# Kernel tuning notes

Measured on AMD Instinct MI355X. Metric: run time of the kernel, lower is better.

## Reference

```python
import jax, jax.numpy as jnp
import numpy as np

T, B, S, D = 512, 32, 512, 512
EPS = 1e-6  # LayerNorm eps


def _ln(x, g, b):
    m = jnp.mean(x, axis=-1, keepdims=True)
    v = jnp.mean((x - m) ** 2, axis=-1, keepdims=True)
    return g * (x - m) * jax.lax.rsqrt(v + EPS) + b


def setup_inputs() -> dict:
    key = jax.random.key(0)
    ks = jax.random.split(key, 10)
    sc = 1.0 / np.sqrt(D).astype(np.float32)
    return {
        "prev_layer": jax.random.normal(ks[0], (T, B, D), jnp.float32),
        "hidden": jax.random.normal(ks[1], (B, D), jnp.float32),
        "enc_output": jax.random.normal(ks[2], (B, S, D), jnp.float32),
        "memory_length": jax.random.randint(ks[3], (B,), 1, S + 1),
        # nn.Linear weights stored as [in, out] (transposed torch layout)
        "W_in": jax.random.normal(ks[4], (D, 3 * D), jnp.float32) * sc,
        "W_enc": jax.random.normal(ks[5], (D, D), jnp.float32) * sc,
        "W_attn_in": jax.random.normal(ks[6], (D, D), jnp.float32) * sc,
        "W_hidden": jax.random.normal(ks[7], (D, D), jnp.float32) * sc,
        "W_ctx": jax.random.normal(ks[8], (D, D), jnp.float32) * sc,
        # LayerNorm gains/biases (5 LNs)
        "g_pre": jnp.ones((3 * D,), jnp.float32), "b_pre": jnp.zeros((3 * D,), jnp.float32),
        "g_enc": jnp.ones((D,), jnp.float32), "b_enc": jnp.zeros((D,), jnp.float32),
        "g_attn": jnp.ones((D,), jnp.float32), "b_attn": jnp.zeros((D,), jnp.float32),
        "g_h": jnp.ones((D,), jnp.float32), "b_h": jnp.zeros((D,), jnp.float32),
        "g_c": jnp.ones((D,), jnp.float32), "b_c": jnp.zeros((D,), jnp.float32),
    }


def reference(prev_layer, hidden, enc_output, W_in, W_enc, W_attn_in, W_hidden,
              W_ctx, g_pre, b_pre, g_enc, b_enc, g_attn, b_attn, g_h, b_h,
              g_c, b_c, memory_length):
    d = prev_layer.shape[-1]
    sqrt_d = jnp.sqrt(jnp.asarray(d, prev_layer.dtype))
    # dropout is identity in eval mode
    preact = _ln(prev_layer @ W_in, g_pre, b_pre)          # [T,B,3D]
    pctx = _ln(enc_output @ W_enc, g_enc, b_enc)           # [B,S,D]
    z, h_gate, pl_t = jnp.split(preact, 3, axis=-1)
    z = jax.nn.sigmoid(z)
    h_gate = jax.nn.sigmoid(h_gate)

    # SRU-style linear recurrence: s_t = (1-z_t)*s_{t-1} + z_t*pl_t
    def step(h, zp):
        z_t, p_t = zp
        s = (1.0 - z_t) * h + z_t * p_t
        return s, s

    hidden_last, ss = jax.lax.scan(step, hidden, (z, pl_t))  # ss: [T,B,D]

    attn_in = _ln(ss @ W_attn_in, g_attn, b_attn)            # [T,B,D]
    align = jnp.einsum('tbd,bsd->bts', attn_in, pctx)        # [B,T,S]
    mask = jnp.arange(pctx.shape[1])[None, :] < memory_length[:, None]  # [B,S]
    align = jnp.where(mask[:, None, :], align, -jnp.inf)
    av = jax.nn.softmax(align / sqrt_d, axis=-1)             # [B,T,S]
    c = jnp.einsum('bts,bsd->tbd', av, pctx)                 # [T,B,D]
    attn_out = c / sqrt_d

    trans = _ln(ss @ W_hidden, g_h, b_h) + _ln(attn_out @ W_ctx, g_c, b_c)
    out = jnp.tanh(trans)
    out = (1.0 - h_gate) * out + h_gate * prev_layer         # [T,B,D]
    p_attn = jnp.transpose(av, (1, 0, 2))                    # [T,B,S]
    return out, hidden_last, p_attn
```

## Files before the change

### kernel.cpp

```cpp
#include <hip/hip_runtime.h>
#include <hip/hip_bf16.h>
#include <cmath>

#define T_ 512
#define B_ 32
#define S_ 512
#define D_ 512
#define NCH 16
#define CT (T_ / NCH)
static constexpr float LN_EPS = 1e-6f;
static constexpr float RSQRT_D = 0.044194173824159216f;

typedef __attribute__((ext_vector_type(8))) __bf16 bf16x8;
typedef __attribute__((ext_vector_type(4))) float f32x4;

struct __align__(8) bfx4 { __hip_bfloat16 x, y, z, w; };
struct __align__(16) u16x8 { unsigned short h[8]; };

__device__ __forceinline__ void g2l16(const void* g, void* l) {
    __builtin_amdgcn_global_load_lds(
        (const __attribute__((address_space(1))) unsigned int*)g,
        (__attribute__((address_space(3))) unsigned int*)l, 16, 0, 0);
}

__device__ __forceinline__ float xr_sum16(float v) {
    v += __shfl_xor(v, 1); v += __shfl_xor(v, 2);
    v += __shfl_xor(v, 4); v += __shfl_xor(v, 8); return v;
}
__device__ __forceinline__ float xr_max16(float v) {
    v = fmaxf(v, __shfl_xor(v, 1)); v = fmaxf(v, __shfl_xor(v, 2));
    v = fmaxf(v, __shfl_xor(v, 4)); v = fmaxf(v, __shfl_xor(v, 8)); return v;
}

__device__ __forceinline__ float sigmoidf_(float x) {
    return 1.f / (1.f + __expf(-x));
}
__device__ __forceinline__ float sigmoid_fast(float x) {
    return __fdividef(1.f, 1.f + __expf(-x));
}
__device__ __forceinline__ float tanh_fast(float x) {
    return 1.f - __fdividef(2.f, __expf(2.f * x) + 1.f);
}
__device__ __forceinline__ float bfu(unsigned short u) {
    unsigned int v = ((unsigned int)u) << 16;
    return __uint_as_float(v);
}
__device__ __forceinline__ unsigned short f2bu(float f) {
    return __hip_bfloat16_raw(__float2bfloat16(f)).x;
}

__device__ __forceinline__ void g128_body(
    const __hip_bfloat16* __restrict__ A, long ldaE,
    const __hip_bfloat16* __restrict__ Bw,
    __hip_bfloat16* __restrict__ out, long outStrideB,
    float2* __restrict__ part, int partMul, int partBase,
    float scale, int bx, int by)
{
    __shared__ char smem[32768];
    const int m0 = by * 128, n0 = bx * 128;
    const int tid = threadIdx.x, lane = tid & 63, w = tid >> 6;
    const int wm = (w >> 1) * 64, wn = (w & 1) * 64;
    const int srow = lane >> 2, skB = (lane & 3) * 16;
    const int q = lane >> 4, c = lane & 15;

    f32x4 acc[4][4];
#pragma unroll
    for (int i = 0; i < 4; i++)
#pragma unroll
        for (int j = 0; j < 4; j++) acc[i][j] = (f32x4)(0.0f);

    const char* ga0 = (const char*)(A + (long)(m0 + w * 16 + srow) * ldaE) + skB;
    const char* ga1 = (const char*)(A + (long)(m0 + (w + 4) * 16 + srow) * ldaE) + skB;
    const char* gb0 = (const char*)(Bw + (long)(n0 + w * 16 + srow) * 512) + skB;
    const char* gb1 = (const char*)(Bw + (long)(n0 + (w + 4) * 16 + srow) * 512) + skB;
    char* la0 = smem + w * 1024 + lane * 16;
    char* la1 = smem + (w + 4) * 1024 + lane * 16;
    char* lb0 = smem + 8192 + w * 1024 + lane * 16;
    char* lb1 = smem + 8192 + (w + 4) * 1024 + lane * 16;
    const char* Ar = smem + (wm + c) * 64 + q * 16;
    const char* Br = smem + 8192 + (wn + c) * 64 + q * 16;

    g2l16(ga0, la0);
    g2l16(ga1, la1);
    g2l16(gb0, lb0);
    g2l16(gb1, lb1);
    __syncthreads();

#pragma unroll
    for (int kk = 0; kk < 16; kk++) {
        const int cb = (kk & 1) << 14;
        const int nb = cb ^ 16384;
        if (kk < 15) {
            const long kb = (long)(kk + 1) * 64;
            g2l16(ga0 + kb, la0 + nb);
            g2l16(ga1 + kb, la1 + nb);
            g2l16(gb0 + kb, lb0 + nb);
            g2l16(gb1 + kb, lb1 + nb);
        }
        bf16x8 af[4], bfr[4];
#pragma unroll
        for (int i = 0; i < 4; i++) {
            af[i] = *(const bf16x8*)(Ar + cb + i * 1024);
            bfr[i] = *(const bf16x8*)(Br + cb + i * 1024);
        }
#pragma unroll
        for (int i = 0; i < 4; i++)
#pragma unroll
            for (int j = 0; j < 4; j++)
                acc[i][j] = __builtin_amdgcn_mfma_f32_16x16x32_bf16(
                    af[i], bfr[j], acc[i][j], 0, 0, 0);
        __syncthreads();
    }

    if (part) {
        float2* sred = (float2*)smem;
#pragma unroll
        for (int i = 0; i < 4; i++)
#pragma unroll
            for (int r = 0; r < 4; r++) {
                float s = 0.f, qq = 0.f;
#pragma unroll
                for (int j = 0; j < 4; j++) {
                    float v = acc[i][j][r] * scale; s += v; qq += v * v;
                }
                s = xr_sum16(s); qq = xr_sum16(qq);
                if (c == 0) sred[(wm + i * 16 + q * 4 + r) * 2 + (w & 1)] =
                    make_float2(s, qq);
            }
        __syncthreads();
        if ((w & 1) == 0 && c == 0) {
#pragma unroll
            for (int i = 0; i < 4; i++)
#pragma unroll
                for (int r = 0; r < 4; r++) {
                    int row = wm + i * 16 + q * 4 + r;
                    float2 a = sred[row * 2], b2 = sred[row * 2 + 1];
                    part[(long)bx * 16384 + (long)(m0 + row) * partMul + partBase] =
                        make_float2(a.x + b2.x, a.y + b2.y);
                }
        }
        __syncthreads();
    }

    for (int p = 0; p < 2; p++) {
        if ((w >> 1) == p) {
#pragma unroll
            for (int i = 0; i < 4; i++)
#pragma unroll
                for (int j = 0; j < 4; j++)
#pragma unroll
                    for (int r = 0; r < 4; r++) {
                        int row = i * 16 + q * 4 + r;
                        int col = wn + j * 16 + c;
                        ((__hip_bfloat16*)smem)[row * 128 + col] =
                            __float2bfloat16(acc[i][j][r] * scale);
                    }
        }
        __syncthreads();
#pragma unroll
        for (int rnd = 0; rnd < 4; rnd++) {
            int row = rnd * 16 + (tid >> 4);
            int ch = tid & 15;
            uint4 v = *(const uint4*)(smem + row * 256 + ch * 16);
            long grow = m0 + p * 64 + row;
            *(uint4*)((char*)out + grow * outStrideB + (long)n0 * 2 + ch * 16) = v;
        }
        __syncthreads();
    }
}

__global__ __launch_bounds__(256) void g128(
    const __hip_bfloat16* __restrict__ A, long ldaE,
    const __hip_bfloat16* __restrict__ Bw, long bStrideZ,
    __hip_bfloat16* __restrict__ out, long outStrideB,
    float2* __restrict__ part, float scale, int swizzle)
{
    int bx, by, pmul = 1, pbase = 0;
    if (gridDim.z > 1) {
        const int bpz = gridDim.x * gridDim.y;
        const int nwg = bpz * gridDim.z;
        const int lin = (blockIdx.z * gridDim.y + blockIdx.y) * gridDim.x
                        + blockIdx.x;
        const int swz = (lin & 7) * (nwg >> 3) + (lin >> 3);
        const int z = swz / bpz, rem = swz % bpz;
        bx = rem % gridDim.x; by = rem / gridDim.x;
        A += (long)z * 512;
        Bw += (long)z * bStrideZ;
        out += (long)z * 512;
        pmul = 32; pbase = z;
    } else if (swizzle) {
        const int nwg = gridDim.x * gridDim.y;
        const int lin = blockIdx.y * gridDim.x + blockIdx.x;
        const int cpx = nwg >> 3;
        const int swz = (lin & 7) * cpx + (lin >> 3);
        bx = swz % gridDim.x; by = swz / gridDim.x;
    } else { bx = blockIdx.x; by = blockIdx.y; }
    g128_body(A, ldaE, Bw, out, outStrideB, part, pmul, pbase, scale, bx, by);
}

__global__ __launch_bounds__(256) void g128e2s(
    const __hip_bfloat16* __restrict__ encb,
    const __hip_bfloat16* __restrict__ WE2,
    __hip_bfloat16* __restrict__ E2, float2* __restrict__ partA,
    const __hip_bfloat16* __restrict__ preb, const float2* __restrict__ stats,
    const float* __restrict__ gpre, const float* __restrict__ bpre,
    float* __restrict__ Ap, float* __restrict__ Bp)
{
    const int bid = blockIdx.x;
    if (bid < 512) {
        int i2 = (bid & 31) * 256 + threadIdx.x;
        int b = i2 >> 8, d = (i2 & 255) * 2;
        int idx = b * 512 + d;
        int ch = bid >> 5;
        float2 gz = *(const float2*)(gpre + d), bz = *(const float2*)(bpre + d);
        float2 gp = *(const float2*)(gpre + 1024 + d);
        float2 bp = *(const float2*)(bpre + 1024 + d);
        float A0 = 1.f, s0 = 0.f, A1 = 1.f, s1 = 0.f;
        for (int t = ch * CT; t < (ch + 1) * CT; t++) {
            long row = (long)t * 32 + b;
            float2 st = stats[row];
            ushort2 zr = *(const ushort2*)(preb + row * 1536 + d);
            ushort2 pr = *(const ushort2*)(preb + row * 1536 + 1024 + d);
            float z0 = sigmoidf_((bfu(zr.x) - st.x) * st.y * gz.x + bz.x);
            float z1 = sigmoidf_((bfu(zr.y) - st.x) * st.y * gz.y + bz.y);
            float p0 = (bfu(pr.x) - st.x) * st.y * gp.x + bp.x;
            float p1 = (bfu(pr.y) - st.x) * st.y * gp.y + bp.y;
            A0 *= (1.f - z0); s0 = (1.f - z0) * s0 + z0 * p0;
            A1 *= (1.f - z1); s1 = (1.f - z1) * s1 + z1 * p1;
        }
        *(float2*)(Ap + ch * 16384 + idx) = make_float2(A0, A1);
        *(float2*)(Bp + ch * 16384 + idx) = make_float2(s0, s1);
        return;
    }
    const int local = bid - 512;
    const int swz = (local & 7) * 128 + (local >> 3);
    g128_body(encb, 512, WE2, E2, 2048, partA, 1, 0, 1.f, swz & 7, swz >> 3);
}

__global__ __launch_bounds__(256) void mfix3(
    const __hip_bfloat16* __restrict__ preb, const float2* __restrict__ stats,
    const float* __restrict__ gpre, const float* __restrict__ bpre,
    const float* __restrict__ sinb, __hip_bfloat16* __restrict__ ssb,
    const __hip_bfloat16* __restrict__ E2,
    __hip_bfloat16* __restrict__ pctxb, __hip_bfloat16* __restrict__ pwT,
    const float2* __restrict__ partA,
    const float* __restrict__ g, const float* __restrict__ bb,
    const float* __restrict__ uv)
{
    __shared__ __hip_bfloat16 t[32][34];
    __shared__ float2 sst[32];
    const int bid = blockIdx.x;
    if (bid < 512) {
        int i2 = (bid & 31) * 256 + threadIdx.x;
        int b = i2 >> 8, d = (i2 & 255) * 2;
        int idx = b * 512 + d;
        int ch = bid >> 5;
        float2 gz = *(const float2*)(gpre + d), bz = *(const float2*)(bpre + d);
        float2 gp = *(const float2*)(gpre + 1024 + d);
        float2 bp = *(const float2*)(bpre + 1024 + d);
        float2 sv = *(const float2*)(sinb + ch * 16384 + idx);
        float s0 = sv.x, s1 = sv.y;
        for (int tt = ch * CT; tt < (ch + 1) * CT; tt++) {
            long row = (long)tt * 32 + b;
            float2 st = stats[row];
            ushort2 zr = *(const ushort2*)(preb + row * 1536 + d);
            ushort2 pr = *(const ushort2*)(preb + row * 1536 + 1024 + d);
            float z0 = sigmoidf_((bfu(zr.x) - st.x) * st.y * gz.x + bz.x);
            float z1 = sigmoidf_((bfu(zr.y) - st.x) * st.y * gz.y + bz.y);
            float p0 = (bfu(pr.x) - st.x) * st.y * gp.x + bp.x;
            float p1 = (bfu(pr.y) - st.x) * st.y * gp.y + bp.y;
            s0 += z0 * (p0 - s0);
            s1 += z1 * (p1 - s1);
            ushort2 o;
            o.x = f2bu(s0); o.y = f2bu(s1);
            *(ushort2*)(ssb + (long)tt * 16384 + idx) = o;
        }
        return;
    }
    const int local = bid - 512;
    const int d0 = (local & 15) * 32;
    const int s0 = ((local >> 4) & 15) * 32;
    const int b = local >> 8;
    if (threadIdx.x < 32) {
        long row = (long)b * 512 + s0 + threadIdx.x;
        float s = 0.f, qq = 0.f;
#pragma unroll
        for (int cb = 0; cb < 4; cb++) {
            float2 v = partA[(long)cb * 16384 + row]; s += v.x; qq += v.y;
        }
        float mn = s * (1.f / 512);
        sst[threadIdx.x] =
            make_float2(mn, rsqrtf(qq * (1.f / 512) - mn * mn + LN_EPS));
    }
    __syncthreads();
    const int tx = threadIdx.x & 31, ty = threadIdx.x >> 5;
    const float gv = g[d0 + tx], bv = bb[d0 + tx];
    const float ud = uv[d0 + tx], vd = uv[512 + d0 + tx];
#pragma unroll
    for (int i = 0; i < 4; i++) {
        int srow = s0 + ty + i * 8;
        long row = (long)b * 512 + srow;
        float2 s = sst[ty + i * 8];
        float pc = __bfloat162float(E2[row * 1024 + d0 + tx]);
        pctxb[row * 512 + d0 + tx] =
            __float2bfloat16((pc - s.x) * s.y * gv + bv);
        float pr = __bfloat162float(E2[row * 1024 + 512 + d0 + tx]);
        t[ty + i * 8][tx] = __float2bfloat16(s.y * pr - s.y * s.x * ud + vd);
    }
    __syncthreads();
#pragma unroll
    for (int i = 0; i < 4; i++)
        pwT[(long)b * 262144 + (long)(d0 + ty + i * 8) * 512 + s0 + tx] =
            t[tx][ty + i * 8];
}

#define RC_BUF 34816
__global__ __launch_bounds__(256, 2) void gemm_attn(
    const __hip_bfloat16* __restrict__ attninC2,
    const __hip_bfloat16* __restrict__ pctxb,
    const float2* __restrict__ partB,
    const float* __restrict__ g_att, const float* __restrict__ b_att,
    const int* __restrict__ mlen,
    float* __restrict__ pattn, __hip_bfloat16* __restrict__ softb)
{
    __shared__ char smem[74240];
    float2* sst = (float2*)(smem + 69632);
    float* gln = (float*)(smem + 69888);
    float* bln = (float*)(smem + 71936);
    const int lin = blockIdx.z * 16 + blockIdx.y;
    const int swzb = (lin & 7) * 64 + (lin >> 3);
    const int b = swzb >> 4;
    const long t0 = (long)(swzb & 15) * 32;
    const int tid = threadIdx.x, lane = tid & 63, w = tid >> 6;

    if (tid < 32) {
        long grow = (t0 + tid) * 32 + b;
        float s = 0.f, qq = 0.f;
#pragma unroll
        for (int cb = 0; cb < 4; cb++) {
            float2 v = partB[(long)cb * 16384 + grow]; s += v.x; qq += v.y;
        }
        float mn = s * (1.f / 512);
        sst[tid] = make_float2(mn, rsqrtf(qq * (1.f / 512) - mn * mn + LN_EPS));
    }
    gln[tid] = g_att[tid]; gln[256 + tid] = g_att[256 + tid];
    bln[tid] = b_att[tid]; bln[256 + tid] = b_att[256 + tid];

    f32x4 acc[2][8];
#pragma unroll
    for (int m = 0; m < 2; m++)
#pragma unroll
        for (int j = 0; j < 8; j++) acc[m][j] = (f32x4)(0.0f);

    const __hip_bfloat16* A = attninC2 + (long)b * 1024 + t0 * 32768;
    const __hip_bfloat16* Bm = pctxb + (long)b * 262144;
    const char* ga = (const char*)(A + (long)(w * 16 + (lane >> 2)) * 32768) + (lane & 3) * 16;
    char* la = smem + w * 1024 + lane * 16;
    const char* gb = (const char*)(Bm + (long)(w * 128 + (lane >> 2)) * 512) + (lane & 3) * 16;
    char* lb = smem + 2048 + w * 8192 + lane * 16;
    const long ldbB16 = 512L * 32;
    const char* Ar = smem + (lane & 15) * 64 + (lane >> 4) * 16;
    const char* Br = smem + 2048 + (w * 128 + (lane & 15)) * 64 + (lane >> 4) * 16;

    if (w < 2) g2l16(ga, la);
#pragma unroll
    for (int s = 0; s < 8; s++) g2l16(gb + s * ldbB16, lb + s * 1024);
    __syncthreads();

    const int fr = lane & 15, kq = lane >> 4;
    const float2 st0 = sst[fr], st1 = sst[16 + fr];

#pragma unroll
    for (int kk = 0; kk < 16; kk++) {
        const int cb = (kk & 1) * RC_BUF;
        const int nb = ((kk & 1) ^ 1) * RC_BUF;
        if (kk < 15) {
            const long kb = (long)(kk + 1) * 64;
            if (w < 2) g2l16(ga + kb, la + nb);
#pragma unroll
            for (int s = 0; s < 8; s++)
                g2l16(gb + kb + s * ldbB16, lb + nb + s * 1024);
        }
        bf16x8 af[2], bfr[8];
#pragma unroll
        for (int m = 0; m < 2; m++) af[m] = *(const bf16x8*)(Ar + cb + m * 1024);
#pragma unroll
        for (int j = 0; j < 8; j++) bfr[j] = *(const bf16x8*)(Br + cb + j * 1024);
        {
            const int k0 = kk * 32 + kq * 8;
            float4 gq0 = *(const float4*)(gln + k0);
            float4 gq1 = *(const float4*)(gln + k0 + 4);
            float4 bq0 = *(const float4*)(bln + k0);
            float4 bq1 = *(const float4*)(bln + k0 + 4);
            float gj[8] = {gq0.x, gq0.y, gq0.z, gq0.w, gq1.x, gq1.y, gq1.z, gq1.w};
            float bj[8] = {bq0.x, bq0.y, bq0.z, bq0.w, bq1.x, bq1.y, bq1.z, bq1.w};
            u16x8 u0 = __builtin_bit_cast(u16x8, af[0]);
            u16x8 u1 = __builtin_bit_cast(u16x8, af[1]);
#pragma unroll
            for (int j = 0; j < 8; j++) {
                u0.h[j] = f2bu((bfu(u0.h[j]) - st0.x) * st0.y * gj[j] + bj[j]);
                u1.h[j] = f2bu((bfu(u1.h[j]) - st1.x) * st1.y * gj[j] + bj[j]);
            }
            af[0] = __builtin_bit_cast(bf16x8, u0);
            af[1] = __builtin_bit_cast(bf16x8, u1);
        }
#pragma unroll
        for (int m = 0; m < 2; m++)
#pragma unroll
            for (int j = 0; j < 8; j++)
                acc[m][j] = __builtin_amdgcn_mfma_f32_16x16x32_bf16(
                    af[m], bfr[j], acc[m][j], 0, 0, 0);
        __syncthreads();
    }

    const int q = lane >> 4, c = lane & 15;
    const int len = mlen[b];
    float* sred = (float*)smem;

#pragma unroll
    for (int m = 0; m < 2; m++)
#pragma unroll
        for (int r = 0; r < 4; r++) {
            float mx = -INFINITY;
#pragma unroll
            for (int j = 0; j < 8; j++) {
                int col = w * 128 + j * 16 + c;
                float v = acc[m][j][r] * RSQRT_D;
                acc[m][j][r] = v;
                if (col < len) mx = fmaxf(mx, v);
            }
            mx = xr_max16(mx);
            if (c == 0) sred[(m * 16 + q * 4 + r) * 4 + w] = mx;
        }
    __syncthreads();
    float rmax[2][4];
#pragma unroll
    for (int m = 0; m < 2; m++)
#pragma unroll
        for (int r = 0; r < 4; r++) {
            int row = m * 16 + q * 4 + r;
            rmax[m][r] = fmaxf(fmaxf(sred[row * 4], sred[row * 4 + 1]),
                               fmaxf(sred[row * 4 + 2], sred[row * 4 + 3]));
        }
    __syncthreads();
#pragma unroll
    for (int m = 0; m < 2; m++)
#pragma unroll
        for (int r = 0; r < 4; r++) {
            float s = 0.f;
#pragma unroll
            for (int j = 0; j < 8; j++) {
                int col = w * 128 + j * 16 + c;
                float e = (col < len) ? __expf(acc[m][j][r] - rmax[m][r]) : 0.f;
                acc[m][j][r] = e; s += e;
            }
            s = xr_sum16(s);
            if (c == 0) sred[(m * 16 + q * 4 + r) * 4 + w] = s;
        }
    __syncthreads();
    float rinv[2][4];
#pragma unroll
    for (int m = 0; m < 2; m++)
#pragma unroll
        for (int r = 0; r < 4; r++) {
            int row = m * 16 + q * 4 + r;
            rinv[m][r] = 1.f / (sred[row * 4] + sred[row * 4 + 1] +
                                sred[row * 4 + 2] + sred[row * 4 + 3]);
        }
    __syncthreads();

#pragma unroll
    for (int m = 0; m < 2; m++)
#pragma unroll
        for (int j = 0; j < 8; j++)
#pragma unroll
            for (int r = 0; r < 4; r++) {
                int row = m * 16 + q * 4 + r;
                int col = w * 128 + j * 16 + c;
                float p = acc[m][j][r] * rinv[m][r];
                pattn[((t0 + row) * 32 + b) * 512 + col] = p;
                ((__hip_bfloat16*)smem)[row * 512 + col] = __float2bfloat16(p);
            }
    __syncthreads();
#pragma unroll
    for (int rnd = 0; rnd < 8; rnd++) {
        int row = rnd * 4 + w;
        uint4 v = *(const uint4*)(smem + row * 1024 + lane * 16);
        *(uint4*)((char*)softb + ((t0 + row) * 32 + b) * 1024 + lane * 16) = v;
    }
}

__global__ __launch_bounds__(256) void fin_ep(
    const __hip_bfloat16* __restrict__ h2r,
    const __hip_bfloat16* __restrict__ C2,
    const __hip_bfloat16* __restrict__ preb,
    const float2* __restrict__ partC,
    const float2* __restrict__ partH,
    const float2* __restrict__ st_p,
    const float* __restrict__ g_c, const float* __restrict__ b_c,
    const float* __restrict__ g_h, const float* __restrict__ b_h,
    const float* __restrict__ g_pre, const float* __restrict__ b_pre,
    const float* __restrict__ prev, float* __restrict__ out)
{
    __shared__ float2 shc[32], shh[32];
    const long m0 = (long)blockIdx.x * 32;
    const int tid = threadIdx.x;
    if (tid < 32) {
        long rowg = m0 + tid;
        float s = 0.f, qq = 0.f;
#pragma unroll
        for (int cb = 0; cb < 4; cb++) {
            float2 v = partC[(long)cb * 16384 + rowg]; s += v.x; qq += v.y;
        }
        float mn = s * (1.f / 512);
        shc[tid] = make_float2(mn, rsqrtf(qq * (1.f / 512) - mn * mn + LN_EPS));
    } else if (tid < 64) {
        long rowg = m0 + tid - 32;
        float s = 0.f, qq = 0.f;
#pragma unroll
        for (int cb = 0; cb < 4; cb++) {
            float2 v = partH[(long)cb * 16384 + rowg]; s += v.x; qq += v.y;
        }
        float mn = s * (1.f / 512);
        shh[tid - 32] = make_float2(mn, rsqrtf(qq * (1.f / 512) - mn * mn + LN_EPS));
    }
    __syncthreads();
#pragma unroll
    for (int ch = 0; ch < 16; ch++) {
        int f4 = ch * 256 + tid;
        int row = f4 >> 7;
        long rowg = m0 + row;
        int col = (f4 & 127) * 4;
        ushort4 h2 = *(const ushort4*)((const char*)h2r + rowg * 1024 + col * 2);
        ushort4 h1 = *(const ushort4*)((const char*)C2 + rowg * 2048 + 1024 + col * 2);
        ushort4 hr = *(const ushort4*)((const char*)preb + rowg * 3072 + 1024 + col * 2);
        float4 pv = *(const float4*)(prev + rowg * 512 + col);
        float4 gc = *(const float4*)(g_c + col), bc = *(const float4*)(b_c + col);
        float4 gh = *(const float4*)(g_h + col), bh = *(const float4*)(b_h + col);
        float4 gp = *(const float4*)(g_pre + 512 + col);
        float4 bp = *(const float4*)(b_pre + 512 + col);
        float2 sc = shc[row], sh = shh[row], sp = st_p[rowg];
        auto fuse = [&](unsigned short h2u, unsigned short h1u, unsigned short hru,
                        float pvv, float gcv, float bcv, float ghv, float bhv,
                        float gpv, float bpv) -> float {
            float t2 = (bfu(h2u) - sc.x) * sc.y * gcv + bcv;
            float t1 = (bfu(h1u) - sh.x) * sh.y * ghv + bhv;
            float hg = sigmoid_fast((bfu(hru) - sp.x) * sp.y * gpv + bpv);
            return (1.f - hg) * tanh_fast(t1 + t2) + hg * pvv;
        };
        float4 o;
        o.x = fuse(h2.x, h1.x, hr.x, pv.x, gc.x, bc.x, gh.x, bh.x, gp.x, bp.x);
        o.y = fuse(h2.y, h1.y, hr.y, pv.y, gc.y, bc.y, gh.y, bh.y, gp.y, bp.y);
        o.z = fuse(h2.z, h1.z, hr.z, pv.z, gc.z, bc.z, gh.z, bh.z, gp.z, bp.z);
        o.w = fuse(h2.w, h1.w, hr.w, pv.w, gc.w, bc.w, gh.w, bh.w, gp.w, bp.w);
        *(float4*)(out + rowg * 512 + col) = o;
    }
}

__global__ __launch_bounds__(256) void cvt4d(
    const float* __restrict__ a, __hip_bfloat16* __restrict__ ya,
    const float* __restrict__ b, __hip_bfloat16* __restrict__ yb)
{
    int i = blockIdx.x * 256 + threadIdx.x;
    const float* x; __hip_bfloat16* y; int k;
    if (i < 2097152) { x = a; y = ya; k = i; }
    else { x = b; y = yb; k = i - 2097152; }
    float4 v = ((const float4*)x)[k];
    bfx4 o;
    o.x = __float2bfloat16(v.x); o.y = __float2bfloat16(v.y);
    o.z = __float2bfloat16(v.z); o.w = __float2bfloat16(v.w);
    ((bfx4*)y)[k] = o;
}

__global__ __launch_bounds__(256) void wtrans(
    const float* __restrict__ w0, const float* __restrict__ w1,
    const float* __restrict__ w2, const float* __restrict__ w3,
    const float* __restrict__ w4, __hip_bfloat16* __restrict__ WT,
    __hip_bfloat16* __restrict__ WE2)
{
    int z = blockIdx.z;
    const float* W; __hip_bfloat16* O; int N;
    if (z == 0)      { W = w0; O = WT;                          N = 1536; }
    else if (z == 1) { W = w1; O = WE2;                         N = 512; }
    else if (z == 2) { W = w2; O = WT + 786432 + 262144;        N = 512; }
    else if (z == 3) { W = w3; O = WT + 786432 + 524288;        N = 512; }
    else             { W = w4; O = WT + 786432 + 786432;        N = 512; }
    int n0 = blockIdx.x * 32, k0 = blockIdx.y * 32;
    if (n0 >= N) return;
    __shared__ float t[32][33];
    int tx = threadIdx.x & 31, ty = threadIdx.x >> 5;
#pragma unroll
    for (int i = 0; i < 4; i++)
        t[ty + i * 8][tx] = W[(long)(k0 + ty + i * 8) * N + n0 + tx];
    __syncthreads();
#pragma unroll
    for (int i = 0; i < 4; i++)
        O[(long)(n0 + ty + i * 8) * 512 + k0 + tx] =
            __float2bfloat16(t[tx][ty + i * 8]);
}

__global__ __launch_bounds__(256) void wprep(
    const __hip_bfloat16* __restrict__ wctxT, const float* __restrict__ g,
    __hip_bfloat16* __restrict__ wgT,
    const float* __restrict__ Wenc, __hip_bfloat16* __restrict__ wencb,
    const float* __restrict__ Wctx, const float* __restrict__ bvec,
    float* __restrict__ uv)
{
    const int bid = blockIdx.x;
    if (bid < 1024) {
        int i = bid * 256 + threadIdx.x;
        int d1 = i & 511;
        wgT[i] = __float2bfloat16(__bfloat162float(wctxT[i]) * g[d1]);
    } else if (bid < 1280) {
        int i = (bid - 1024) * 256 + threadIdx.x;
        float4 v = ((const float4*)Wenc)[i];
        bfx4 o;
        o.x = __float2bfloat16(v.x); o.y = __float2bfloat16(v.y);
        o.z = __float2bfloat16(v.z); o.w = __float2bfloat16(v.w);
        ((bfx4*)wencb)[i] = o;
    } else {
        int d = (bid - 1280) * 256 + threadIdx.x;
        float u = 0.f, v = 0.f;
        for (int k = 0; k < 512; k++) {
            float w = Wctx[(long)k * 512 + d];
            u += g[k] * w; v += bvec[k] * w;
        }
        uv[d] = u; uv[512 + d] = v;
    }
}

__global__ __launch_bounds__(256) void stats_fin(
    const float2* __restrict__ part, float2* __restrict__ stats)
{
    int r = blockIdx.x * 256 + threadIdx.x;
    float s = 0.f, qq = 0.f;
#pragma unroll
    for (int cb = 0; cb < 12; cb++) {
        float2 v = part[(long)cb * 16384 + r]; s += v.x; qq += v.y;
    }
    float m = s * (1.f / 1536);
    float rs = rsqrtf(qq * (1.f / 1536) - m * m + LN_EPS);
    stats[r] = make_float2(m, rs);
}

__global__ __launch_bounds__(256) void scan_part2(
    const float* __restrict__ Ap, const float* __restrict__ Bp,
    const float* __restrict__ h0, float* __restrict__ sin_,
    float* __restrict__ hlast)
{
    int idx = blockIdx.x * 256 + threadIdx.x;
    float s = h0[idx];
    for (int ch = 0; ch < NCH; ch++) {
        sin_[ch * 16384 + idx] = s;
        s = Ap[ch * 16384 + idx] * s + Bp[ch * 16384 + idx];
    }
    hlast[idx] = s;
}

extern "C" void kernel_launch(void* const* d_in, const int* in_sizes, int n_in,
                              void* d_out, int out_size, void* d_ws, size_t ws_size,
                              hipStream_t stream) {
    const float* prev  = (const float*)d_in[0];
    const float* hid0  = (const float*)d_in[1];
    const float* enc   = (const float*)d_in[2];
    const int*   mlen  = (const int*)  d_in[3];
    const float* W_in  = (const float*)d_in[4];
    const float* W_enc = (const float*)d_in[5];
    const float* W_att = (const float*)d_in[6];
    const float* W_hid = (const float*)d_in[7];
    const float* W_ctx = (const float*)d_in[8];
    const float* g_pre = (const float*)d_in[9];
    const float* b_pre = (const float*)d_in[10];
    const float* g_enc = (const float*)d_in[11];
    const float* b_enc = (const float*)d_in[12];
    const float* g_att = (const float*)d_in[13];
    const float* b_att = (const float*)d_in[14];
    const float* g_h   = (const float*)d_in[15];
    const float* b_h   = (const float*)d_in[16];
    const float* g_c   = (const float*)d_in[17];
    const float* b_c   = (const float*)d_in[18];

    float* out   = (float*)d_out;
    float* hlast = out + (long)T_ * B_ * D_;
    float* pattn = hlast + (long)B_ * D_;

    char* ws = (char*)d_ws;
    __hip_bfloat16* preb    = (__hip_bfloat16*)(ws);
    __hip_bfloat16* WT      = (__hip_bfloat16*)(ws + 50331648);
    __hip_bfloat16* prevb   = (__hip_bfloat16*)(ws + 54525952);
    __hip_bfloat16* encb    = (__hip_bfloat16*)(ws + 71303168);
    __hip_bfloat16* pctxb   = (__hip_bfloat16*)(ws + 88080384);
    __hip_bfloat16* pwT     = (__hip_bfloat16*)(ws + 104857600);
    __hip_bfloat16* ssb     = (__hip_bfloat16*)(ws + 121634816);
    __hip_bfloat16* C2      = (__hip_bfloat16*)(ws + 138412032);
    __hip_bfloat16* E2      = (__hip_bfloat16*)(ws + 171966464);
    __hip_bfloat16* softb   = (__hip_bfloat16*)(ws + 171966464);
    __hip_bfloat16* h2raw   = (__hip_bfloat16*)(ws + 188743680);
    float2* part            = (float2*)(ws + 205520896);
    float2* stats           = (float2*)(ws + 207618048);
    float* scanA            = (float*)(ws + 207749120);
    float* scanB            = (float*)(ws + 208797696);
    float* sinb             = (float*)(ws + 209846272);
    __hip_bfloat16* WE2     = (__hip_bfloat16*)(ws + 211419136);
    float* uv               = (float*)(ws + 212467712);
    __hip_bfloat16* WgT     = (__hip_bfloat16*)scanA;
    __hip_bfloat16* Wencbf  = (__hip_bfloat16*)scanB;

    float2* partA = part;
    float2* partB = part + 8 * 16384;
    float2* partC = part;

    const __hip_bfloat16* W_attT = WT + 786432 + 262144;
    const __hip_bfloat16* W_ctxT = WT + 786432 + 786432;

    dim3 blk(256);

    cvt4d<<<16384, blk, 0, stream>>>(prev, prevb, enc, encb);
    wtrans<<<dim3(48, 16, 5), blk, 0, stream>>>(W_in, W_enc, W_att, W_hid,
                                                W_ctx, WT, WE2);
    wprep<<<1282, blk, 0, stream>>>(W_ctxT, g_enc, WgT, W_enc, Wencbf,
                                    W_ctx, b_enc, uv);
    g128<<<dim3(4, 4), blk, 0, stream>>>(WgT, 512, Wencbf, 0, WE2 + 262144,
                                         1024, nullptr, 1.f, 0);

    g128<<<dim3(12, 128), blk, 0, stream>>>(prevb, 512, WT, 0, preb, 3072,
                                            part, 1.f, 1);
    stats_fin<<<64, blk, 0, stream>>>(part, stats);

    g128e2s<<<1536, blk, 0, stream>>>(encb, WE2, E2, partA, preb, stats,
                                      g_pre, b_pre, scanA, scanB);
    scan_part2<<<64, blk, 0, stream>>>(scanA, scanB, hid0, sinb, hlast);

    mfix3<<<8704, blk, 0, stream>>>(preb, stats, g_pre, b_pre, sinb, ssb,
                                    E2, pctxb, pwT, partA, g_enc, b_enc, uv);

    g128<<<dim3(8, 128), blk, 0, stream>>>(ssb, 512, W_attT, 0, C2, 2048,
                                           partB, 1.f, 1);

    gemm_attn<<<dim3(1, 16, 32), blk, 0, stream>>>(C2, pctxb, partB,
                                                   g_att, b_att, mlen,
                                                   pattn, softb);

    g128<<<dim3(4, 4, 32), blk, 0, stream>>>(softb, 16384, pwT, 262144,
                                             h2raw, 32768, partC, RSQRT_D, 0);

    fin_ep<<<512, blk, 0, stream>>>(h2raw, C2, preb, partC,
                                    partB + 4 * 16384, stats,
                                    g_c, b_c, g_h, b_h, g_pre, b_pre, prev,
                                    out);
}
```

Baseline: 421.6 us.

## Enlarge attention GEMM tile to 64 rows with 512-thread blocks sharing B

The fused attention-score/softmax kernel now processes 64 time rows per block with 8 waves instead of 32 rows with 4 waves. Two wave groups share each staged pctx K-slice, so the global B-operand traffic per output row is halved. The block count drops from 512 to 256 and shared memory per block grows, which lowers occupancy to one block per CU and reduces latency hiding.

```diff
diff --git a/kernel.cpp b/kernel.cpp
--- a/kernel.cpp
+++ b/kernel.cpp
@@ -314,8 +314,8 @@
             t[tx][ty + i * 8];
 }
 
-#define RC_BUF 34816
-__global__ __launch_bounds__(256, 2) void gemm_attn(
+#define AT_BUF 36864
+__global__ __launch_bounds__(512, 1) void gemm_attn(
     const __hip_bfloat16* __restrict__ attninC2,
     const __hip_bfloat16* __restrict__ pctxb,
     const float2* __restrict__ partB,
@@ -323,17 +323,19 @@
     const int* __restrict__ mlen,
     float* __restrict__ pattn, __hip_bfloat16* __restrict__ softb)
 {
-    __shared__ char smem[74240];
-    float2* sst = (float2*)(smem + 69632);
-    float* gln = (float*)(smem + 69888);
-    float* bln = (float*)(smem + 71936);
-    const int lin = blockIdx.z * 16 + blockIdx.y;
-    const int swzb = (lin & 7) * 64 + (lin >> 3);
-    const int b = swzb >> 4;
-    const long t0 = (long)(swzb & 15) * 32;
+    __shared__ char smem[78336];
+    float2* sst = (float2*)(smem + 73728);
+    float* gln = (float*)(smem + 74240);
+    float* bln = (float*)(smem + 76288);
+    const int lin = blockIdx.z * 8 + blockIdx.y;
+    const int swzb = (lin & 7) * 32 + (lin >> 3);
+    const int b = swzb >> 3;
+    const long t0 = (long)(swzb & 7) * 64;
     const int tid = threadIdx.x, lane = tid & 63, w = tid >> 6;
-
-    if (tid < 32) {
+    const int wg = w >> 2;
+    const int wq = w & 3;
+
+    if (tid < 64) {
         long grow = (t0 + tid) * 32 + b;
         float s = 0.f, qq = 0.f;
 #pragma unroll
@@ -343,8 +345,10 @@
         float mn = s * (1.f / 512);
         sst[tid] = make_float2(mn, rsqrtf(qq * (1.f / 512) - mn * mn + LN_EPS));
     }
-    gln[tid] = g_att[tid]; gln[256 + tid] = g_att[256 + tid];
-    bln[tid] = b_att[tid]; bln[256 + tid] = b_att[256 + tid];
+    if (tid < 256) {
+        gln[tid] = g_att[tid]; gln[256 + tid] = g_att[256 + tid];
+        bln[tid] = b_att[tid]; bln[256 + tid] = b_att[256 + tid];
+    }
 
     f32x4 acc[2][8];
 #pragma unroll
@@ -354,31 +358,34 @@
 
     const __hip_bfloat16* A = attninC2 + (long)b * 1024 + t0 * 32768;
     const __hip_bfloat16* Bm = pctxb + (long)b * 262144;
-    const char* ga = (const char*)(A + (long)(w * 16 + (lane >> 2)) * 32768) + (lane & 3) * 16;
-    char* la = smem + w * 1024 + lane * 16;
-    const char* gb = (const char*)(Bm + (long)(w * 128 + (lane >> 2)) * 512) + (lane & 3) * 16;
-    char* lb = smem + 2048 + w * 8192 + lane * 16;
+    const int awl = w & 3;
+    const char* ga = (const char*)(A + (long)(wg * 32 + awl * 16 + (lane >> 2)) * 32768)
+                     + (lane & 3) * 16;
+    char* la = smem + wg * 2048 + awl * 1024 + lane * 16;
+    const int doA = (awl < 2);
+    const char* gb = (const char*)(Bm + (long)(w * 64 + (lane >> 2)) * 512) + (lane & 3) * 16;
+    char* lb = smem + 4096 + w * 4096 + lane * 16;
     const long ldbB16 = 512L * 32;
-    const char* Ar = smem + (lane & 15) * 64 + (lane >> 4) * 16;
-    const char* Br = smem + 2048 + (w * 128 + (lane & 15)) * 64 + (lane >> 4) * 16;
-
-    if (w < 2) g2l16(ga, la);
-#pragma unroll
-    for (int s = 0; s < 8; s++) g2l16(gb + s * ldbB16, lb + s * 1024);
+    const char* Ar = smem + wg * 2048 + (lane & 15) * 64 + (lane >> 4) * 16;
+    const char* Br = smem + 4096 + (wq * 128 + (lane & 15)) * 64 + (lane >> 4) * 16;
+
+    if (doA) g2l16(ga, la);
+#pragma unroll
+    for (int s = 0; s < 4; s++) g2l16(gb + s * ldbB16, lb + s * 1024);
     __syncthreads();
 
     const int fr = lane & 15, kq = lane >> 4;
-    const float2 st0 = sst[fr], st1 = sst[16 + fr];
+    const float2 st0 = sst[wg * 32 + fr], st1 = sst[wg * 32 + 16 + fr];
 
 #pragma unroll
     for (int kk = 0; kk < 16; kk++) {
-        const int cb = (kk & 1) * RC_BUF;
-        const int nb = ((kk & 1) ^ 1) * RC_BUF;
+        const int cb = (kk & 1) * AT_BUF;
+        const int nb = ((kk & 1) ^ 1) * AT_BUF;
         if (kk < 15) {
             const long kb = (long)(kk + 1) * 64;
-            if (w < 2) g2l16(ga + kb, la + nb);
-#pragma unroll
-            for (int s = 0; s < 8; s++)
+            if (doA) g2l16(ga + kb, la + nb);
+#pragma unroll
+            for (int s = 0; s < 4; s++)
                 g2l16(gb + kb + s * ldbB16, lb + nb + s * 1024);
         }
         bf16x8 af[2], bfr[8];
@@ -416,6 +423,7 @@
     const int q = lane >> 4, c = lane & 15;
     const int len = mlen[b];
     float* sred = (float*)smem;
+    const int rb = wg * 32;
 
 #pragma unroll
     for (int m = 0; m < 2; m++)
@@ -424,13 +432,13 @@
             float mx = -INFINITY;
 #pragma unroll
             for (int j = 0; j < 8; j++) {
-                int col = w * 128 + j * 16 + c;
+                int col = wq * 128 + j * 16 + c;
                 float v = acc[m][j][r] * RSQRT_D;
                 acc[m][j][r] = v;
                 if (col < len) mx = fmaxf(mx, v);
             }
             mx = xr_max16(mx);
-            if (c == 0) sred[(m * 16 + q * 4 + r) * 4 + w] = mx;
+            if (c == 0) sred[(rb + m * 16 + q * 4 + r) * 4 + wq] = mx;
         }
     __syncthreads();
     float rmax[2][4];
@@ -438,7 +446,7 @@
     for (int m = 0; m < 2; m++)
 #pragma unroll
         for (int r = 0; r < 4; r++) {
-            int row = m * 16 + q * 4 + r;
+            int row = rb + m * 16 + q * 4 + r;
             rmax[m][r] = fmaxf(fmaxf(sred[row * 4], sred[row * 4 + 1]),
                                fmaxf(sred[row * 4 + 2], sred[row * 4 + 3]));
         }
@@ -450,12 +458,12 @@
             float s = 0.f;
 #pragma unroll
             for (int j = 0; j < 8; j++) {
-                int col = w * 128 + j * 16 + c;
+                int col = wq * 128 + j * 16 + c;
                 float e = (col < len) ? __expf(acc[m][j][r] - rmax[m][r]) : 0.f;
                 acc[m][j][r] = e; s += e;
             }
             s = xr_sum16(s);
-            if (c == 0) sred[(m * 16 + q * 4 + r) * 4 + w] = s;
+            if (c == 0) sred[(rb + m * 16 + q * 4 + r) * 4 + wq] = s;
         }
     __syncthreads();
     float rinv[2][4];
@@ -463,7 +471,7 @@
     for (int m = 0; m < 2; m++)
 #pragma unroll
         for (int r = 0; r < 4; r++) {
-            int row = m * 16 + q * 4 + r;
+            int row = rb + m * 16 + q * 4 + r;
             rinv[m][r] = 1.f / (sred[row * 4] + sred[row * 4 + 1] +
                                 sred[row * 4 + 2] + sred[row * 4 + 3]);
         }
@@ -475,8 +483,8 @@
         for (int j = 0; j < 8; j++)
 #pragma unroll
             for (int r = 0; r < 4; r++) {
-                int row = m * 16 + q * 4 + r;
-                int col = w * 128 + j * 16 + c;
+                int row = rb + m * 16 + q * 4 + r;
+                int col = wq * 128 + j * 16 + c;
                 float p = acc[m][j][r] * rinv[m][r];
                 pattn[((t0 + row) * 32 + b) * 512 + col] = p;
                 ((__hip_bfloat16*)smem)[row * 512 + col] = __float2bfloat16(p);
@@ -484,7 +492,7 @@
     __syncthreads();
 #pragma unroll
     for (int rnd = 0; rnd < 8; rnd++) {
-        int row = rnd * 4 + w;
+        int row = rnd * 8 + (tid >> 6);
         uint4 v = *(const uint4*)(smem + row * 1024 + lane * 16);
         *(uint4*)((char*)softb + ((t0 + row) * 32 + b) * 1024 + lane * 16) = v;
     }
@@ -737,9 +745,9 @@
     g128<<<dim3(8, 128), blk, 0, stream>>>(ssb, 512, W_attT, 0, C2, 2048,
                                            partB, 1.f, 1);
 
-    gemm_attn<<<dim3(1, 16, 32), blk, 0, stream>>>(C2, pctxb, partB,
-                                                   g_att, b_att, mlen,
-                                                   pattn, softb);
+    gemm_attn<<<dim3(1, 8, 32), dim3(512), 0, stream>>>(C2, pctxb, partB,
+                                                        g_att, b_att, mlen,
+                                                        pattn, softb);
 
     g128<<<dim3(4, 4, 32), blk, 0, stream>>>(softb, 16384, pwT, 262144,
                                              h2raw, 32768, partC, RSQRT_D, 0);
```

Result: faster. 411.6 us (-2.4%).
